# Performance work log

Hardware: AMD Instinct MI355X
Metric: run time of the kernel (lower is better)

The kernel has to match this reference:

```python
import jax, jax.numpy as jnp
import numpy as np

N_NODES = 50000
N_EDGES = 800000
N_REL = 8
DIM = 256


def setup_inputs() -> dict:
    key = jax.random.key(0)
    ks = jax.random.split(key, 6)
    x = jax.random.normal(ks[0], (N_NODES, DIM), dtype=jnp.float32)
    # xavier-uniform-ish scale for [R, in, out] weights
    limit = float(np.sqrt(6.0 / (DIM + DIM)))
    W0 = jax.random.uniform(ks[1], (N_REL, DIM, DIM), dtype=jnp.float32, minval=-limit, maxval=limit)
    W1 = jax.random.uniform(ks[2], (N_REL, DIM, DIM), dtype=jnp.float32, minval=-limit, maxval=limit)
    b0 = jnp.zeros((DIM,), dtype=jnp.float32)
    b1 = jnp.zeros((DIM,), dtype=jnp.float32)
    edge_index = jax.random.randint(ks[3], (2, N_EDGES), 0, N_NODES, dtype=jnp.int64)
    edge_type = jax.random.randint(ks[4], (N_EDGES,), 0, N_REL, dtype=jnp.int64)
    return {"x": x, "W0": W0, "b0": b0, "W1": W1, "b1": b1,
            "edge_index": edge_index, "edge_type": edge_type}


def _rgcn_layer(x, W, b, src, dst, edge_type, num_nodes):
    # grouped GEMM over all relations: [R, N, out]
    xt = jnp.einsum('ni,rio->rno', x, W)
    # per-edge message = relu(x[src] @ W[edge_type] + b)  -> [E, out]
    msg = jax.nn.relu(xt[edge_type, src] + b)
    # scatter-add into destination nodes
    return jax.ops.segment_sum(msg, dst, num_segments=num_nodes)


def reference(x, W0, b0, W1, b1, edge_index, edge_type):
    src, dst = edge_index[0], edge_index[1]
    h = _rgcn_layer(x, W0, b0, src, dst, edge_type, x.shape[0])
    h = _rgcn_layer(h, W1, b1, src, dst, edge_type, x.shape[0])
    return h
```

## Files before the change

### kernel.cpp

```cpp
#include <hip/hip_runtime.h>

#define DIM 256
#define N_REL 8

typedef __attribute__((ext_vector_type(8))) short short8_t;
typedef __attribute__((ext_vector_type(4))) float float4_t;

__device__ inline unsigned short f2bf(float f) {
    unsigned u = __float_as_uint(f);
    u += 0x7FFFu + ((u >> 16) & 1u);
    return (unsigned short)(u >> 16);
}
__device__ inline float bf2f(unsigned short h) {
    return __uint_as_float(((unsigned)h) << 16);
}

__global__ __launch_bounds__(256) void cast_f32_bf16(
    const float* __restrict__ in, unsigned short* __restrict__ out, int n4)
{
    const int i = blockIdx.x * blockDim.x + threadIdx.x;
    if (i >= n4) return;
    const float4 v = ((const float4*)in)[i];
    ushort4 o;
    o.x = f2bf(v.x); o.y = f2bf(v.y); o.z = f2bf(v.z); o.w = f2bf(v.w);
    ((ushort4*)out)[i] = o;
}

__global__ __launch_bounds__(256) void transpose_cast_w(
    const float* __restrict__ W, unsigned short* __restrict__ Wt)
{
    __shared__ float tile[32][33];
    const int rel = blockIdx.z;
    const int i0 = blockIdx.x * 32, o0 = blockIdx.y * 32;
    const int tx = threadIdx.x, ty = threadIdx.y;
    const float* Wr = W + (size_t)rel * DIM * DIM;
    unsigned short* Wtr = Wt + (size_t)rel * DIM * DIM;
#pragma unroll
    for (int j = 0; j < 4; j++)
        tile[ty + 8 * j][tx] = Wr[(size_t)(i0 + ty + 8 * j) * DIM + o0 + tx];
    __syncthreads();
#pragma unroll
    for (int j = 0; j < 4; j++)
        Wtr[(size_t)(o0 + ty + 8 * j) * DIM + i0 + tx] = f2bf(tile[tx][ty + 8 * j]);
}

__global__ __launch_bounds__(256) void gemm_mfma_bias_relu(
    const unsigned short* __restrict__ Xb,
    const unsigned short* __restrict__ Wtb,
    const float* __restrict__ bias,
    unsigned short* __restrict__ Yall, int M, int Rtiles)
{
    __shared__ __align__(16) short smem[24576];

    const unsigned L = blockIdx.x;
    const int xcd = L & 7;
    const unsigned g = L >> 3;
    const int combo = g & 15;
    const int rt = (int)((g >> 4) << 3) | xcd;
    if (rt >= Rtiles) return;
    const int m0 = rt * 128;
    const int n0 = (combo & 1) * 128;
    const int rel = combo >> 1;

    const unsigned short* Wt = Wtb + (size_t)rel * DIM * DIM;
    unsigned short* Y = Yall + (size_t)rel * M * DIM;

    const int t = threadIdx.x;
    const int lane = t & 63;
    const int w = t >> 6;
    const int wr = w & 1, wc = w >> 1;
    const int r = lane & 15, q = lane >> 4;

    const int sl = lane & 3;
    const int rsub = lane >> 2;
    const unsigned short* gA[2];
    const unsigned short* gB[2];
#pragma unroll
    for (int h = 0; h < 2; h++) {
        const int row = h * 64 + w * 16 + rsub;
        const int gseg = sl ^ ((row >> 1) & 3);
        gA[h] = Xb + (size_t)(m0 + row) * DIM + gseg * 8;
        gB[h] = Wt + (size_t)(n0 + row) * DIM + gseg * 8;
    }

    const int swz = (q ^ ((r >> 1) & 3)) * 8;
    int offA[4], offB[4];
#pragma unroll
    for (int mi = 0; mi < 4; mi++)
        offA[mi] = (wr * 64 + mi * 16 + r) * 32 + swz;
#pragma unroll
    for (int ni = 0; ni < 4; ni++)
        offB[ni] = (wc * 64 + ni * 16 + r) * 32 + swz;

    float4_t acc[4][4];
#pragma unroll
    for (int i = 0; i < 4; i++)
#pragma unroll
        for (int j = 0; j < 4; j++) {
            float4_t z = {0.f, 0.f, 0.f, 0.f};
            acc[i][j] = z;
        }

#define STAGE(ks, bsel)                                                         \
    {                                                                           \
        const int k0_ = (ks) * 32;                                              \
        short* Ad_ = smem + (bsel) * 8192;                                      \
        short* Bd_ = Ad_ + 4096;                                                \
        _Pragma("unroll")                                                       \
        for (int h = 0; h < 2; h++) {                                           \
            __builtin_amdgcn_global_load_lds(                                   \
                (const __attribute__((address_space(1))) unsigned int*)(gA[h] + k0_), \
                (__attribute__((address_space(3))) unsigned int*)(Ad_ + h * 2048 + w * 512), \
                16, 0, 0);                                                      \
            __builtin_amdgcn_global_load_lds(                                   \
                (const __attribute__((address_space(1))) unsigned int*)(gB[h] + k0_), \
                (__attribute__((address_space(3))) unsigned int*)(Bd_ + h * 2048 + w * 512), \
                16, 0, 0);                                                      \
        }                                                                       \
    }

    STAGE(0, 0);
    STAGE(1, 1);
#pragma unroll
    for (int ks = 0; ks < 8; ks++) {
        if (ks < 6) {
            STAGE(ks + 2, (ks + 2) % 3);
            asm volatile("s_waitcnt vmcnt(8)" ::: "memory");
        } else if (ks == 6) {
            asm volatile("s_waitcnt vmcnt(4)" ::: "memory");
        } else {
            asm volatile("s_waitcnt vmcnt(0)" ::: "memory");
        }
        asm volatile("s_barrier" ::: "memory");

        const short* As_b = smem + (ks % 3) * 8192;
        const short* Bs_b = As_b + 4096;
        short8_t af[4], bf[4];
#pragma unroll
        for (int mi = 0; mi < 4; mi++)
            af[mi] = *(const short8_t*)&As_b[offA[mi]];
#pragma unroll
        for (int ni = 0; ni < 4; ni++)
            bf[ni] = *(const short8_t*)&Bs_b[offB[ni]];
#pragma unroll
        for (int mi = 0; mi < 4; mi++)
#pragma unroll
            for (int ni = 0; ni < 4; ni++)
                acc[mi][ni] = __builtin_amdgcn_mfma_f32_16x16x32_bf16(
                    af[mi], bf[ni], acc[mi][ni], 0, 0, 0);
        asm volatile("s_barrier" ::: "memory");
    }
#undef STAGE

    short* St = smem;

    float bv[4];
#pragma unroll
    for (int ni = 0; ni < 4; ni++)
        bv[ni] = bias[n0 + wc * 64 + ni * 16 + r];

#pragma unroll
    for (int mp = 0; mp < 2; mp++) {
#pragma unroll
        for (int s = 0; s < 2; s++) {
#pragma unroll
            for (int ni = 0; ni < 4; ni++) {
#pragma unroll
                for (int e = 0; e < 4; e++) {
                    const int rl = s * 32 + wr * 16 + q * 4 + e;
                    const int col = wc * 64 + ni * 16 + r;
                    St[rl * 136 + col] =
                        f2bf(fmaxf(acc[mp * 2 + s][ni][e] + bv[ni], 0.f));
                }
            }
        }
        __syncthreads();
#pragma unroll
        for (int j = 0; j < 4; j++) {
            const int id = t + 256 * j;
            const int rl2 = id >> 4;
            const int ch = id & 15;
            const int s = rl2 >> 5;
            const int rl = rl2 & 31;
            const int grow = m0 + (rl >> 4) * 64 + (mp * 2 + s) * 16 + (rl & 15);
            const short8_t v = *(const short8_t*)&St[rl2 * 136 + ch * 8];
            if (grow < M)
                *(short8_t*)&Y[(size_t)grow * DIM + n0 + ch * 8] = v;
        }
        if (mp == 0) __syncthreads();
    }
}

__global__ __launch_bounds__(256) void count_dst(
    const int* __restrict__ dst, int E, int* __restrict__ cnt)
{
    const int e = blockIdx.x * blockDim.x + threadIdx.x;
    if (e < E) atomicAdd(&cnt[dst[e]], 1);
}

__global__ __launch_bounds__(256) void scan_blocksums(
    const int* __restrict__ cnt, int N, int* __restrict__ bsum)
{
    __shared__ int red[256];
    const int t = threadIdx.x;
    const int base = blockIdx.x * 1024 + t * 4;
    int s = 0;
#pragma unroll
    for (int j = 0; j < 4; j++) {
        const int i = base + j;
        if (i < N) s += cnt[i];
    }
    red[t] = s;
    __syncthreads();
#pragma unroll
    for (int off = 128; off > 0; off >>= 1) {
        if (t < off) red[t] += red[t + off];
        __syncthreads();
    }
    if (t == 0) bsum[blockIdx.x] = red[0];
}

__global__ __launch_bounds__(256) void scan_offsets(
    int* __restrict__ bsum, int nb, int* __restrict__ rowptr, int N)
{
    __shared__ int sh[256];
    const int t = threadIdx.x;
    sh[t] = (t < nb) ? bsum[t] : 0;
    __syncthreads();
    for (int off = 1; off < 256; off <<= 1) {
        const int add = (t >= off) ? sh[t - off] : 0;
        __syncthreads();
        sh[t] += add;
        __syncthreads();
    }
    if (t < nb) bsum[t] = (t == 0) ? 0 : sh[t - 1];
    if (t == 255) rowptr[N] = sh[255];
}

__global__ __launch_bounds__(256) void scan_phase3(
    const int* __restrict__ cnt, int N, const int* __restrict__ bsum,
    int* __restrict__ rowptr, int* __restrict__ cursor)
{
    __shared__ int sh[256];
    const int t = threadIdx.x;
    const int base = blockIdx.x * 1024 + t * 4;
    int v[4];
#pragma unroll
    for (int j = 0; j < 4; j++) {
        const int i = base + j;
        v[j] = (i < N) ? cnt[i] : 0;
    }
    sh[t] = v[0] + v[1] + v[2] + v[3];
    __syncthreads();
    for (int off = 1; off < 256; off <<= 1) {
        const int add = (t >= off) ? sh[t - off] : 0;
        __syncthreads();
        sh[t] += add;
        __syncthreads();
    }
    int run = bsum[blockIdx.x] + ((t == 0) ? 0 : sh[t - 1]);
#pragma unroll
    for (int j = 0; j < 4; j++) {
        const int i = base + j;
        if (i < N) { rowptr[i] = run; cursor[i] = run; }
        run += v[j];
    }
}

__global__ __launch_bounds__(256) void fill_edges(
    const int* __restrict__ src, const int* __restrict__ dst,
    const int* __restrict__ et, int E, int* __restrict__ cursor,
    unsigned* __restrict__ ep)
{
    const int e = blockIdx.x * blockDim.x + threadIdx.x;
    if (e >= E) return;
    const int pos = atomicAdd(&cursor[dst[e]], 1);
    ep[pos] = (unsigned)src[e] | ((unsigned)et[e] << 16);
}

template <typename OT>
__global__ __launch_bounds__(256) void aggregate4(
    const unsigned short* __restrict__ yall,
    const unsigned* __restrict__ ep, const int* __restrict__ rowptr,
    OT* __restrict__ out, int M)
{
    const int lane = threadIdx.x & 63;
    const int half = lane >> 5;
    const int cl = lane & 31;
    const int wv = (blockIdx.x * blockDim.x + threadIdx.x) >> 6;
    const int nw = (gridDim.x * blockDim.x) >> 6;
    const size_t plane = (size_t)M * DIM;

    for (int d = wv; d < M; d += nw) {
        const int beg = rowptr[d], end = rowptr[d + 1];
        float acc[8];
#pragma unroll
        for (int j = 0; j < 8; j++) acc[j] = 0.f;

        for (int c0 = beg; c0 < end; c0 += 64) {
            const int n = min(64, end - c0);
            const unsigned myep = (c0 + lane < end) ? ep[c0 + lane] : 0u;
            for (int i = 0; i < n; i += 8) {
                short8_t u[4];
#pragma unroll
                for (int j = 0; j < 4; j++) {
                    const unsigned p = __shfl(myep, (i + 2 * j + half) & 63);
                    u[j] = *(const short8_t*)(
                        yall + (size_t)(p >> 16) * plane +
                        (size_t)(p & 0xFFFFu) * DIM + cl * 8);
                }
#pragma unroll
                for (int j = 0; j < 4; j++) {
                    if (i + 2 * j + half < n) {
#pragma unroll
                        for (int k = 0; k < 8; k++)
                            acc[k] += bf2f((unsigned short)u[j][k]);
                    }
                }
            }
        }
        float o[8];
#pragma unroll
        for (int j = 0; j < 8; j++)
            o[j] = acc[j] + __shfl(acc[j], (lane + 32) & 63);
        if (lane < 32) {
            OT* dp = out + (size_t)d * DIM + cl * 8;
            if (sizeof(OT) == 4) {
                *(float4*)((float*)dp) = make_float4(o[0], o[1], o[2], o[3]);
                *(float4*)((float*)dp + 4) = make_float4(o[4], o[5], o[6], o[7]);
            } else {
                short8_t v;
#pragma unroll
                for (int j = 0; j < 8; j++) v[j] = (short)f2bf(o[j]);
                *(short8_t*)((unsigned short*)dp) = v;
            }
        }
    }
}

__global__ __launch_bounds__(256) void gemm_bias_relu_f32(
    const float* __restrict__ A, const float* __restrict__ B,
    const float* __restrict__ bias, float* __restrict__ Y, int M)
{
    __shared__ float Asf[16][132];
    __shared__ float Bsf[16][128];
    const int t = threadIdx.x;
    const int tx = t & 15, ty = t >> 4;
    const int row0 = blockIdx.x * 128, col0 = blockIdx.y * 128;
    float acc[8][8];
#pragma unroll
    for (int i = 0; i < 8; i++)
#pragma unroll
        for (int j = 0; j < 8; j++) acc[i][j] = 0.f;
    const int arow = t >> 2, akseg = (t & 3) * 4;
    const int bk0 = t >> 5, bcol = (t & 31) * 4;
    for (int k0 = 0; k0 < DIM; k0 += 16) {
#pragma unroll
        for (int h = 0; h < 2; h++) {
            const int row = row0 + arow + h * 64;
            float4 av = (row < M) ? *(const float4*)(A + (size_t)row * DIM + k0 + akseg)
                                  : make_float4(0, 0, 0, 0);
            Asf[akseg + 0][arow + h * 64] = av.x;
            Asf[akseg + 1][arow + h * 64] = av.y;
            Asf[akseg + 2][arow + h * 64] = av.z;
            Asf[akseg + 3][arow + h * 64] = av.w;
        }
#pragma unroll
        for (int h = 0; h < 2; h++) {
            const int krow = bk0 + h * 8;
            *(float4*)&Bsf[krow][bcol] =
                *(const float4*)(B + (size_t)(k0 + krow) * DIM + col0 + bcol);
        }
        __syncthreads();
#pragma unroll
        for (int k = 0; k < 16; k++) {
            float a[8], b[8];
            *(float4*)&a[0] = *(const float4*)&Asf[k][ty * 4];
            *(float4*)&a[4] = *(const float4*)&Asf[k][64 + ty * 4];
            *(float4*)&b[0] = *(const float4*)&Bsf[k][tx * 4];
            *(float4*)&b[4] = *(const float4*)&Bsf[k][64 + tx * 4];
#pragma unroll
            for (int i = 0; i < 8; i++)
#pragma unroll
                for (int j = 0; j < 8; j++) acc[i][j] = fmaf(a[i], b[j], acc[i][j]);
        }
        __syncthreads();
    }
#pragma unroll
    for (int im = 0; im < 2; im++)
#pragma unroll
        for (int i = 0; i < 4; i++) {
            const int row = row0 + im * 64 + ty * 4 + i;
            if (row >= M) continue;
#pragma unroll
            for (int jm = 0; jm < 2; jm++) {
                const int col = col0 + jm * 64 + tx * 4;
                const float4 bb = *(const float4*)(bias + col);
                float4 o;
                o.x = fmaxf(acc[im * 4 + i][jm * 4 + 0] + bb.x, 0.f);
                o.y = fmaxf(acc[im * 4 + i][jm * 4 + 1] + bb.y, 0.f);
                o.z = fmaxf(acc[im * 4 + i][jm * 4 + 2] + bb.z, 0.f);
                o.w = fmaxf(acc[im * 4 + i][jm * 4 + 3] + bb.w, 0.f);
                *(float4*)(Y + (size_t)row * DIM + col) = o;
            }
        }
}

__global__ __launch_bounds__(256) void scatter_rel(
    const float* __restrict__ y, const int* __restrict__ src,
    const int* __restrict__ dst, const int* __restrict__ et,
    int rel, float* __restrict__ out, int n_edges)
{
    const int lane = threadIdx.x & 63;
    const int wave = (blockIdx.x * blockDim.x + threadIdx.x) >> 6;
    const int nwaves = (gridDim.x * blockDim.x) >> 6;
    for (int e = wave; e < n_edges; e += nwaves) {
        if (et[e] != rel) continue;
        const float4 v = *(const float4*)(y + (size_t)src[e] * DIM + lane * 4);
        float* o = out + (size_t)dst[e] * DIM + lane * 4;
        atomicAdd(o + 0, v.x);
        atomicAdd(o + 1, v.y);
        atomicAdd(o + 2, v.z);
        atomicAdd(o + 3, v.w);
    }
}

static inline size_t align16(size_t x) { return (x + 15) & ~(size_t)15; }

extern "C" void kernel_launch(void* const* d_in, const int* in_sizes, int n_in,
                              void* d_out, int out_size, void* d_ws, size_t ws_size,
                              hipStream_t stream)
{
    const float* x  = (const float*)d_in[0];
    const float* W0 = (const float*)d_in[1];
    const float* b0 = (const float*)d_in[2];
    const float* W1 = (const float*)d_in[3];
    const float* b1 = (const float*)d_in[4];
    const int* eidx = (const int*)d_in[5];
    const int* etyp = (const int*)d_in[6];

    const int M = in_sizes[0] / DIM;
    const int E = in_sizes[6];
    const int* src = eidx;
    const int* dst = eidx + E;
    float* out = (float*)d_out;

    const size_t plane = (size_t)M * DIM;
    const size_t wbytes = (size_t)N_REL * DIM * DIM * 2;

    const size_t need = align16(plane * 2)
                      + align16(plane * 2)
                      + 2 * align16(wbytes)
                      + align16((size_t)(M + 1) * 4)
                      + 2 * align16((size_t)M * 4)
                      + align16((size_t)256 * 4)
                      + align16((size_t)E * 4)
                      + align16((size_t)N_REL * plane * 2);

    if (M < 65536 && ws_size >= need) {
        char* ws = (char*)d_ws;
        size_t off = 0;
        unsigned short* h1b  = (unsigned short*)(ws + off); off = align16(off + plane * 2);
        unsigned short* xb   = (unsigned short*)(ws + off); off = align16(off + plane * 2);
        unsigned short* Wt0b = (unsigned short*)(ws + off); off = align16(off + wbytes);
        unsigned short* Wt1b = (unsigned short*)(ws + off); off = align16(off + wbytes);
        int* rowptr = (int*)(ws + off); off = align16(off + (size_t)(M + 1) * 4);
        int* cnt    = (int*)(ws + off); off = align16(off + (size_t)M * 4);
        int* cursor = (int*)(ws + off); off = align16(off + (size_t)M * 4);
        int* bsum   = (int*)(ws + off); off = align16(off + (size_t)256 * 4);
        unsigned* ep = (unsigned*)(ws + off); off = align16(off + (size_t)E * 4);
        unsigned short* yall = (unsigned short*)(ws + off);

        const int nb = (M + 1023) / 1024;
        hipMemsetAsync(cnt, 0, (size_t)M * 4, stream);
        count_dst<<<(E + 255) / 256, 256, 0, stream>>>(dst, E, cnt);
        scan_blocksums<<<nb, 256, 0, stream>>>(cnt, M, bsum);
        scan_offsets<<<1, 256, 0, stream>>>(bsum, nb, rowptr, M);
        scan_phase3<<<nb, 256, 0, stream>>>(cnt, M, bsum, rowptr, cursor);
        fill_edges<<<(E + 255) / 256, 256, 0, stream>>>(src, dst, etyp, E, cursor, ep);

        cast_f32_bf16<<<(int)((plane / 4 + 255) / 256), 256, 0, stream>>>(
            x, xb, (int)(plane / 4));
        transpose_cast_w<<<dim3(8, 8, N_REL), dim3(32, 8), 0, stream>>>(W0, Wt0b);
        transpose_cast_w<<<dim3(8, 8, N_REL), dim3(32, 8), 0, stream>>>(W1, Wt1b);

        const int Rtiles = (M + 127) / 128;
        const int octets = (Rtiles + 7) / 8;
        const int ggrid = octets * 16 * 8;
        const int agrid = (int)(((size_t)M * 64 + 255) / 256);

        gemm_mfma_bias_relu<<<ggrid, 256, 0, stream>>>(xb, Wt0b, b0, yall, M, Rtiles);
        aggregate4<unsigned short><<<agrid, 256, 0, stream>>>(yall, ep, rowptr, h1b, M);
        gemm_mfma_bias_relu<<<ggrid, 256, 0, stream>>>(h1b, Wt1b, b1, yall, M, Rtiles);
        aggregate4<float><<<agrid, 256, 0, stream>>>(yall, ep, rowptr, out, M);
    } else {
        float* h1 = (float*)d_ws;
        float* y  = (float*)d_ws + plane;
        const dim3 gblk(256), ggrid2((M + 127) / 128, DIM / 128);
        hipMemsetAsync(h1, 0, plane * 4, stream);
        for (int r = 0; r < N_REL; r++) {
            gemm_bias_relu_f32<<<ggrid2, gblk, 0, stream>>>(
                x, W0 + (size_t)r * DIM * DIM, b0, y, M);
            scatter_rel<<<1024, 256, 0, stream>>>(y, src, dst, etyp, r, h1, E);
        }
        hipMemsetAsync(out, 0, plane * 4, stream);
        for (int r = 0; r < N_REL; r++) {
            gemm_bias_relu_f32<<<ggrid2, gblk, 0, stream>>>(
                h1, W1 + (size_t)r * DIM * DIM, b1, y, M);
            scatter_rel<<<1024, 256, 0, stream>>>(y, src, dst, etyp, r, out, E);
        }
    }
}
```

Measured before the change: 508.7 us.

## Fuse prep kernels, merge scans, double-buffer GEMM, aggregate two nodes per wave

Merges the x cast, both weight transposes and the destination count into one launch, and folds the scan-offsets step into the phase-3 scan kernel, which cuts kernel launches. The MFMA GEMM drops from a triple-buffered to a double-buffered LDS pipeline with a non-unrolled k loop, lowering LDS use but shortening load prefetch depth. Aggregation now has each half-wave handle its own destination node and accumulates in double precision, removing the cross-half shuffle reduction. The FP64 accumulation adds costly arithmetic on the hot path.

```diff
diff --git a/kernel.cpp b/kernel.cpp
--- a/kernel.cpp
+++ b/kernel.cpp
@@ -15,33 +15,47 @@
     return __uint_as_float(((unsigned)h) << 16);
 }
 
-__global__ __launch_bounds__(256) void cast_f32_bf16(
-    const float* __restrict__ in, unsigned short* __restrict__ out, int n4)
-{
-    const int i = blockIdx.x * blockDim.x + threadIdx.x;
-    if (i >= n4) return;
-    const float4 v = ((const float4*)in)[i];
-    ushort4 o;
-    o.x = f2bf(v.x); o.y = f2bf(v.y); o.z = f2bf(v.z); o.w = f2bf(v.w);
-    ((ushort4*)out)[i] = o;
-}
-
-__global__ __launch_bounds__(256) void transpose_cast_w(
-    const float* __restrict__ W, unsigned short* __restrict__ Wt)
+__global__ __launch_bounds__(256) void prep_mega(
+    const float* __restrict__ x, unsigned short* __restrict__ xb, int n4,
+    const float* __restrict__ W0, unsigned short* __restrict__ Wt0,
+    const float* __restrict__ W1, unsigned short* __restrict__ Wt1,
+    const int* __restrict__ dst, int E, int* __restrict__ cnt,
+    int nCast, int nW)
 {
     __shared__ float tile[32][33];
-    const int rel = blockIdx.z;
-    const int i0 = blockIdx.x * 32, o0 = blockIdx.y * 32;
-    const int tx = threadIdx.x, ty = threadIdx.y;
-    const float* Wr = W + (size_t)rel * DIM * DIM;
-    unsigned short* Wtr = Wt + (size_t)rel * DIM * DIM;
-#pragma unroll
-    for (int j = 0; j < 4; j++)
-        tile[ty + 8 * j][tx] = Wr[(size_t)(i0 + ty + 8 * j) * DIM + o0 + tx];
-    __syncthreads();
-#pragma unroll
-    for (int j = 0; j < 4; j++)
-        Wtr[(size_t)(o0 + ty + 8 * j) * DIM + i0 + tx] = f2bf(tile[tx][ty + 8 * j]);
+    const int b = blockIdx.x;
+    const int t = threadIdx.x;
+    if (b < nCast) {
+        const int i = b * 256 + t;
+        if (i < n4) {
+            const float4 v = ((const float4*)x)[i];
+            ushort4 o;
+            o.x = f2bf(v.x); o.y = f2bf(v.y); o.z = f2bf(v.z); o.w = f2bf(v.w);
+            ((ushort4*)xb)[i] = o;
+        }
+    } else if (b < nCast + 2 * nW) {
+        const int wi = b - nCast;
+        const float* W = (wi < nW) ? W0 : W1;
+        unsigned short* Wt = (wi < nW) ? Wt0 : Wt1;
+        const int bb = (wi < nW) ? wi : wi - nW;
+        const int rel = bb >> 6;
+        const int bx = bb & 7, by = (bb >> 3) & 7;
+        const int i0 = bx * 32, o0 = by * 32;
+        const int tx = t & 31, ty = t >> 5;
+        const float* Wr = W + (size_t)rel * DIM * DIM;
+        unsigned short* Wtr = Wt + (size_t)rel * DIM * DIM;
+#pragma unroll
+        for (int j = 0; j < 4; j++)
+            tile[ty + 8 * j][tx] = Wr[(size_t)(i0 + ty + 8 * j) * DIM + o0 + tx];
+        __syncthreads();
+#pragma unroll
+        for (int j = 0; j < 4; j++)
+            Wtr[(size_t)(o0 + ty + 8 * j) * DIM + i0 + tx] =
+                f2bf(tile[tx][ty + 8 * j]);
+    } else {
+        const int e = (b - nCast - 2 * nW) * 256 + t;
+        if (e < E) atomicAdd(&cnt[dst[e]], 1);
+    }
 }
 
 __global__ __launch_bounds__(256) void gemm_mfma_bias_relu(
@@ -50,7 +64,7 @@
     const float* __restrict__ bias,
     unsigned short* __restrict__ Yall, int M, int Rtiles)
 {
-    __shared__ __align__(16) short smem[24576];
+    __shared__ __align__(16) short smem[16384];
 
     const unsigned L = blockIdx.x;
     const int xcd = L & 7;
@@ -104,7 +118,7 @@
 #define STAGE(ks, bsel)                                                         \
     {                                                                           \
         const int k0_ = (ks) * 32;                                              \
-        short* Ad_ = smem + (bsel) * 8192;                                      \
+        short* Ad_ = smem + ((bsel) ? 8192 : 0);                                \
         short* Bd_ = Ad_ + 4096;                                                \
         _Pragma("unroll")                                                       \
         for (int h = 0; h < 2; h++) {                                           \
@@ -120,20 +134,18 @@
     }
 
     STAGE(0, 0);
-    STAGE(1, 1);
-#pragma unroll
+#pragma unroll 1
     for (int ks = 0; ks < 8; ks++) {
-        if (ks < 6) {
-            STAGE(ks + 2, (ks + 2) % 3);
-            asm volatile("s_waitcnt vmcnt(8)" ::: "memory");
-        } else if (ks == 6) {
+        const int cur = ks & 1;
+        if (ks < 7) {
+            STAGE(ks + 1, cur ^ 1);
             asm volatile("s_waitcnt vmcnt(4)" ::: "memory");
         } else {
             asm volatile("s_waitcnt vmcnt(0)" ::: "memory");
         }
         asm volatile("s_barrier" ::: "memory");
 
-        const short* As_b = smem + (ks % 3) * 8192;
+        const short* As_b = smem + (cur ? 8192 : 0);
         const short* Bs_b = As_b + 4096;
         short8_t af[4], bf[4];
 #pragma unroll
@@ -191,13 +203,6 @@
     }
 }
 
-__global__ __launch_bounds__(256) void count_dst(
-    const int* __restrict__ dst, int E, int* __restrict__ cnt)
-{
-    const int e = blockIdx.x * blockDim.x + threadIdx.x;
-    if (e < E) atomicAdd(&cnt[dst[e]], 1);
-}
-
 __global__ __launch_bounds__(256) void scan_blocksums(
     const int* __restrict__ cnt, int N, int* __restrict__ bsum)
 {
@@ -220,29 +225,25 @@
     if (t == 0) bsum[blockIdx.x] = red[0];
 }
 
-__global__ __launch_bounds__(256) void scan_offsets(
-    int* __restrict__ bsum, int nb, int* __restrict__ rowptr, int N)
-{
+__global__ __launch_bounds__(256) void scan_write(
+    const int* __restrict__ cnt, int N, const int* __restrict__ bsum, int nb,
+    int* __restrict__ rowptr, int* __restrict__ cursor)
+{
+    __shared__ int sb[64];
     __shared__ int sh[256];
     const int t = threadIdx.x;
-    sh[t] = (t < nb) ? bsum[t] : 0;
+    if (t < 64) sb[t] = (t < nb) ? bsum[t] : 0;
     __syncthreads();
-    for (int off = 1; off < 256; off <<= 1) {
-        const int add = (t >= off) ? sh[t - off] : 0;
-        __syncthreads();
-        sh[t] += add;
-        __syncthreads();
-    }
-    if (t < nb) bsum[t] = (t == 0) ? 0 : sh[t - 1];
-    if (t == 255) rowptr[N] = sh[255];
-}
-
-__global__ __launch_bounds__(256) void scan_phase3(
-    const int* __restrict__ cnt, int N, const int* __restrict__ bsum,
-    int* __restrict__ rowptr, int* __restrict__ cursor)
-{
-    __shared__ int sh[256];
-    const int t = threadIdx.x;
+    for (int off = 1; off < 64; off <<= 1) {
+        int v = 0;
+        if (t < 64) v = sb[t] + ((t >= off) ? sb[t - off] : 0);
+        __syncthreads();
+        if (t < 64) sb[t] = v;
+        __syncthreads();
+    }
+    const int run0 = (blockIdx.x == 0) ? 0 : sb[blockIdx.x - 1];
+    const int total = sb[nb - 1];
+
     const int base = blockIdx.x * 1024 + t * 4;
     int v[4];
 #pragma unroll
@@ -258,13 +259,14 @@
         sh[t] += add;
         __syncthreads();
     }
-    int run = bsum[blockIdx.x] + ((t == 0) ? 0 : sh[t - 1]);
+    int run = run0 + ((t == 0) ? 0 : sh[t - 1]);
 #pragma unroll
     for (int j = 0; j < 4; j++) {
         const int i = base + j;
         if (i < N) { rowptr[i] = run; cursor[i] = run; }
         run += v[j];
     }
+    if ((int)blockIdx.x == nb - 1 && t == 255) rowptr[N] = total;
 }
 
 __global__ __launch_bounds__(256) void fill_edges(
@@ -279,7 +281,7 @@
 }
 
 template <typename OT>
-__global__ __launch_bounds__(256) void aggregate4(
+__global__ __launch_bounds__(256) void aggregate2x(
     const unsigned short* __restrict__ yall,
     const unsigned* __restrict__ ep, const int* __restrict__ rowptr,
     OT* __restrict__ out, int M)
@@ -290,48 +292,51 @@
     const int wv = (blockIdx.x * blockDim.x + threadIdx.x) >> 6;
     const int nw = (gridDim.x * blockDim.x) >> 6;
     const size_t plane = (size_t)M * DIM;
-
-    for (int d = wv; d < M; d += nw) {
-        const int beg = rowptr[d], end = rowptr[d + 1];
-        float acc[8];
-#pragma unroll
-        for (int j = 0; j < 8; j++) acc[j] = 0.f;
-
-        for (int c0 = beg; c0 < end; c0 += 64) {
-            const int n = min(64, end - c0);
-            const unsigned myep = (c0 + lane < end) ? ep[c0 + lane] : 0u;
-            for (int i = 0; i < n; i += 8) {
+    const int npair = (M + 1) >> 1;
+
+    for (int pr = wv; pr < npair; pr += nw) {
+        const int d = 2 * pr + half;
+        const bool live = (d < M);
+        double acc[8];
+#pragma unroll
+        for (int j = 0; j < 8; j++) acc[j] = 0.0;
+
+        int beg = 0, end = 0;
+        if (live) { beg = rowptr[d]; end = rowptr[d + 1]; }
+
+        for (int c0 = beg; c0 < end; c0 += 32) {
+            const int n = min(32, end - c0);
+            const unsigned myep = (c0 + cl < end) ? ep[c0 + cl] : 0u;
+            for (int i = 0; i < n; i += 4) {
                 short8_t u[4];
 #pragma unroll
                 for (int j = 0; j < 4; j++) {
-                    const unsigned p = __shfl(myep, (i + 2 * j + half) & 63);
+                    const unsigned p = __shfl(myep, half * 32 + ((i + j) & 31));
                     u[j] = *(const short8_t*)(
                         yall + (size_t)(p >> 16) * plane +
                         (size_t)(p & 0xFFFFu) * DIM + cl * 8);
                 }
 #pragma unroll
                 for (int j = 0; j < 4; j++) {
-                    if (i + 2 * j + half < n) {
+                    if (i + j < n) {
 #pragma unroll
                         for (int k = 0; k < 8; k++)
-                            acc[k] += bf2f((unsigned short)u[j][k]);
+                            acc[k] += (double)bf2f((unsigned short)u[j][k]);
                     }
                 }
             }
         }
-        float o[8];
-#pragma unroll
-        for (int j = 0; j < 8; j++)
-            o[j] = acc[j] + __shfl(acc[j], (lane + 32) & 63);
-        if (lane < 32) {
+        if (live) {
             OT* dp = out + (size_t)d * DIM + cl * 8;
             if (sizeof(OT) == 4) {
-                *(float4*)((float*)dp) = make_float4(o[0], o[1], o[2], o[3]);
-                *(float4*)((float*)dp + 4) = make_float4(o[4], o[5], o[6], o[7]);
+                *(float4*)((float*)dp) = make_float4(
+                    (float)acc[0], (float)acc[1], (float)acc[2], (float)acc[3]);
+                *(float4*)((float*)dp + 4) = make_float4(
+                    (float)acc[4], (float)acc[5], (float)acc[6], (float)acc[7]);
             } else {
                 short8_t v;
 #pragma unroll
-                for (int j = 0; j < 8; j++) v[j] = (short)f2bf(o[j]);
+                for (int j = 0; j < 8; j++) v[j] = (short)f2bf((float)acc[j]);
                 *(short8_t*)((unsigned short*)dp) = v;
             }
         }
@@ -471,28 +476,29 @@
         unsigned* ep = (unsigned*)(ws + off); off = align16(off + (size_t)E * 4);
         unsigned short* yall = (unsigned short*)(ws + off);
 
+        const int n4 = (int)(plane / 4);
+        const int nCast = (n4 + 255) / 256;
+        const int nW = 512;
+        const int nCnt = (E + 255) / 256;
+        hipMemsetAsync(cnt, 0, (size_t)M * 4, stream);
+        prep_mega<<<nCast + 2 * nW + nCnt, 256, 0, stream>>>(
+            x, xb, n4, W0, Wt0b, W1, Wt1b, dst, E, cnt, nCast, nW);
+
         const int nb = (M + 1023) / 1024;
-        hipMemsetAsync(cnt, 0, (size_t)M * 4, stream);
-        count_dst<<<(E + 255) / 256, 256, 0, stream>>>(dst, E, cnt);
         scan_blocksums<<<nb, 256, 0, stream>>>(cnt, M, bsum);
-        scan_offsets<<<1, 256, 0, stream>>>(bsum, nb, rowptr, M);
-        scan_phase3<<<nb, 256, 0, stream>>>(cnt, M, bsum, rowptr, cursor);
+        scan_write<<<nb, 256, 0, stream>>>(cnt, M, bsum, nb, rowptr, cursor);
         fill_edges<<<(E + 255) / 256, 256, 0, stream>>>(src, dst, etyp, E, cursor, ep);
-
-        cast_f32_bf16<<<(int)((plane / 4 + 255) / 256), 256, 0, stream>>>(
-            x, xb, (int)(plane / 4));
-        transpose_cast_w<<<dim3(8, 8, N_REL), dim3(32, 8), 0, stream>>>(W0, Wt0b);
-        transpose_cast_w<<<dim3(8, 8, N_REL), dim3(32, 8), 0, stream>>>(W1, Wt1b);
 
         const int Rtiles = (M + 127) / 128;
         const int octets = (Rtiles + 7) / 8;
         const int ggrid = octets * 16 * 8;
-        const int agrid = (int)(((size_t)M * 64 + 255) / 256);
+        const int npair = (M + 1) / 2;
+        const int agrid = (npair * 64 + 255) / 256;
 
         gemm_mfma_bias_relu<<<ggrid, 256, 0, stream>>>(xb, Wt0b, b0, yall, M, Rtiles);
-        aggregate4<unsigned short><<<agrid, 256, 0, stream>>>(yall, ep, rowptr, h1b, M);
+        aggregate2x<unsigned short><<<agrid, 256, 0, stream>>>(yall, ep, rowptr, h1b, M);
         gemm_mfma_bias_relu<<<ggrid, 256, 0, stream>>>(h1b, Wt1b, b1, yall, M, Rtiles);
-        aggregate4<float><<<agrid, 256, 0, stream>>>(yall, ep, rowptr, out, M);
+        aggregate2x<float><<<agrid, 256, 0, stream>>>(yall, ep, rowptr, out, M);
     } else {
         float* h1 = (float*)d_ws;
         float* y  = (float*)d_ws + plane;
```

Result: faster. 497.4 us (-2.2%).
